# Performance work log

Measured on AMD Instinct MI355X. Metric: run time of the kernel, lower is better.

## Reference

```python
import jax, jax.numpy as jnp
import numpy as np

NUM_HEADS = 4
SPATIAL_DS = 2
EPS = 1e-5


def setup_inputs() -> dict:
    key = jax.random.key(0)
    ks = jax.random.split(key, 6)
    B, C, H, W = 8, 256, 64, 64
    hd = C // NUM_HEADS
    return {
        "x": jax.random.normal(ks[0], (B, C, H, W), jnp.float32),
        "gn_w": jnp.ones((C,), jnp.float32),
        "gn_b": jnp.zeros((C,), jnp.float32),
        "wq": jax.random.normal(ks[1], (C, C), jnp.float32) * (C ** -0.5),
        "wk": jax.random.normal(ks[2], (hd, C), jnp.float32) * (C ** -0.5),
        "wv": jax.random.normal(ks[3], (hd, C), jnp.float32) * (C ** -0.5),
        "wo": jax.random.normal(ks[4], (C, C), jnp.float32) * (C ** -0.5),
        "gamma": jnp.full((C,), 1e-4, jnp.float32),
    }


def reference(x, gn_w, gn_b, wq, wk, wv, wo, gamma):
    B, C, H, W = x.shape
    hd = C // NUM_HEADS
    scale = hd ** -0.5
    ds = SPATIAL_DS

    # GroupNorm with 1 group: normalize over (C,H,W) per sample, per-channel affine
    mu = jnp.mean(x, axis=(1, 2, 3), keepdims=True)
    var = jnp.var(x, axis=(1, 2, 3), keepdims=True)
    xn = (x - mu) * jax.lax.rsqrt(var + EPS)
    xn = xn * gn_w[None, :, None, None] + gn_b[None, :, None, None]

    # Q projection (1x1 conv == channel matmul): (B, heads, N, hd)
    q = jnp.einsum('oc,bchw->bohw', wq, xn).reshape(B, NUM_HEADS, hd, H * W)
    q = jnp.swapaxes(q, 2, 3)  # (B, h, N, hd)

    # AvgPool2d(ds, ds) on normalized input for K/V
    Hd, Wd = H // ds, W // ds
    x_ds = xn.reshape(B, C, Hd, ds, Wd, ds).mean(axis=(3, 5))

    k = jnp.einsum('oc,bchw->bohw', wk, x_ds).reshape(B, hd, Hd * Wd)
    k = jnp.swapaxes(k, 1, 2)  # (B, M, hd) single shared head
    v = jnp.einsum('oc,bchw->bohw', wv, x_ds).reshape(B, hd, Hd * Wd)
    v = jnp.swapaxes(v, 1, 2)  # (B, M, hd)

    # Multi-query attention: queries per-head, shared K/V
    attn = jnp.einsum('bhnd,bmd->bhnm', q, k) * scale
    attn = jax.nn.softmax(attn, axis=-1)
    out = jnp.einsum('bhnm,bmd->bhnd', attn, v)  # (B, h, N, hd)

    out = jnp.swapaxes(out, 2, 3).reshape(B, C, H, W)
    out = jnp.einsum('oc,bchw->bohw', wo, out)

    return x + out * gamma[None, :, None, None]
```

## Files before the change

### kernel.cpp

```cpp
#include <hip/hip_runtime.h>


#define CNT_INV (1.0f/1048576.0f)
#define EPSV 1e-5f
#define QSCALE 0.18033688f

#define WS_STATS 0
#define WS_XNT   64
#define WS_K     5242944
#define WS_V     5505088
#define WS_WQB   5767232
#define WS_WKV   5800000
#define WS_WOB   5816384

typedef __attribute__((ext_vector_type(8))) short bf8_t;
typedef __attribute__((ext_vector_type(4))) float f4_t;

static __device__ __forceinline__ unsigned fbits(float f) {
  union { float f; unsigned u; } v; v.f = f; return v.u;
}
static __device__ __forceinline__ unsigned short f2bf(float f) {
  unsigned u = fbits(f);
  return (unsigned short)((u + 0x7fffu + ((u >> 16) & 1u)) >> 16);
}
static __device__ __forceinline__ unsigned pk_rnd(float a, float b) {
  return __builtin_amdgcn_perm(fbits(b) + 0x8000u, fbits(a) + 0x8000u, 0x07060302u);
}
static __device__ __forceinline__ unsigned pk_tr(float a, float b) {
  return __builtin_amdgcn_perm(fbits(b), fbits(a), 0x07060302u);
}
static __device__ __forceinline__ float bf2f(unsigned short h) {
  union { unsigned u; float f; } v; v.u = ((unsigned)h) << 16; return v.f;
}
static __device__ __forceinline__ float fexp2(float x) {
  float r; asm("v_exp_f32 %0, %1" : "=v"(r) : "v"(x)); return r;
}

static __device__ __forceinline__ bf8_t affine8(bf8_t r, const float* a8, const float* b8) {
  union { bf8_t v; unsigned short u[8]; unsigned w[4]; } in, out;
  in.v = r;
#pragma unroll
  for (int i = 0; i < 4; ++i) {
    float lo = fmaf(bf2f(in.u[2 * i]),     a8[2 * i],     b8[2 * i]);
    float hi = fmaf(bf2f(in.u[2 * i + 1]), a8[2 * i + 1], b8[2 * i + 1]);
    out.w[i] = pk_rnd(lo, hi);
  }
  return out.v;
}

static __device__ __forceinline__ bf8_t pool_affine(bf8_t s00, bf8_t s01, bf8_t s10, bf8_t s11,
                                                    const float* a4, const float* b8) {
  union { bf8_t v; unsigned short u[8]; unsigned w[4]; } x00, x01, x10, x11, out;
  x00.v = s00; x01.v = s01; x10.v = s10; x11.v = s11;
#pragma unroll
  for (int i = 0; i < 4; ++i) {
    float lo = (bf2f(x00.u[2 * i]) + bf2f(x01.u[2 * i])) +
               (bf2f(x10.u[2 * i]) + bf2f(x11.u[2 * i]));
    float hi = (bf2f(x00.u[2 * i + 1]) + bf2f(x01.u[2 * i + 1])) +
               (bf2f(x10.u[2 * i + 1]) + bf2f(x11.u[2 * i + 1]));
    lo = fmaf(lo, a4[2 * i],     b8[2 * i]);
    hi = fmaf(hi, a4[2 * i + 1], b8[2 * i + 1]);
    out.w[i] = pk_rnd(lo, hi);
  }
  return out.v;
}

__global__ __launch_bounds__(256) void k_prep(const float* __restrict__ x,
                                              const float* __restrict__ wq,
                                              const float* __restrict__ wk,
                                              const float* __restrict__ wv,
                                              const float* __restrict__ wo,
                                              float* __restrict__ stats,
                                              unsigned short* __restrict__ wqb,
                                              unsigned short* __restrict__ wkvb,
                                              unsigned short* __restrict__ wob,
                                              unsigned short* __restrict__ xtb) {
  __shared__ unsigned short T[128][72];
  __shared__ float red[8];
  const int blk = blockIdx.x;
  const int t = threadIdx.x;
  if (blk < 512) {
    const int b = blk >> 6;
    const int chunk = blk & 63;
    const float4* xb = (const float4*)(x + (size_t)b * 1048576 + (size_t)chunk * 16384);
    float s = 0.f, s2 = 0.f;
#pragma unroll
    for (int it = 0; it < 16; ++it) {
      float4 v = xb[it * 256 + t];
      s  += v.x + v.y + v.z + v.w;
      s2 += v.x * v.x + v.y * v.y + v.z * v.z + v.w * v.w;
    }
#pragma unroll
    for (int o = 32; o > 0; o >>= 1) {
      s  += __shfl_down(s, o);
      s2 += __shfl_down(s2, o);
    }
    const int wid = t >> 6;
    if ((t & 63) == 0) { red[wid] = s; red[4 + wid] = s2; }
    __syncthreads();
    if (t == 0) {
      atomicAdd(&stats[b * 2 + 0], red[0] + red[1] + red[2] + red[3]);
      atomicAdd(&stats[b * 2 + 1], red[4] + red[5] + red[6] + red[7]);
    }
  } else if (blk < 1152) {
    const int idx = (blk - 512) * 256 + t;
    if (idx < 65536) wqb[idx] = f2bf(wq[idx]);
    else if (idx < 81920) wkvb[idx - 65536] = f2bf(wk[idx - 65536]);
    else if (idx < 98304) wkvb[idx - 65536] = f2bf(wv[idx - 81920]);
    else if (idx < 163840) wob[idx - 98304] = f2bf(wo[idx - 98304]);
  } else {
    const int idx = blk - 1152;
    const int hp = idx & 31, cq = (idx >> 5) & 3, b = idx >> 7;
    const int c0 = cq * 64, n0 = hp * 128;
    const int n4 = (t & 31) * 4, cl = t >> 5;
    const int wswz = t & 7;
#pragma unroll
    for (int p = 0; p < 8; ++p) {
      const int c = c0 + p * 8 + cl;
      const int pc = (p ^ wswz) * 8 + cl;
      float4 v = *(const float4*)&x[(size_t)(b * 256 + c) * 4096 + n0 + n4];
      T[n4 + 0][pc] = f2bf(v.x);
      T[n4 + 1][pc] = f2bf(v.y);
      T[n4 + 2][pc] = f2bf(v.z);
      T[n4 + 3][pc] = f2bf(v.w);
    }
    __syncthreads();
    {
      const int r = t >> 1, cb4 = (t & 1) * 4;
      const int rswz = (t >> 3) & 7;
      unsigned short* dst = xtb + ((size_t)b * 4096 + n0 + r) * 256 + c0 + cb4 * 8;
#pragma unroll
      for (int u = 0; u < 4; ++u)
        *(uint4*)(dst + u * 8) = *(const uint4*)&T[r][((cb4 + u) ^ rswz) * 8];
    }
  }
}

__global__ __launch_bounds__(256) void k_gemm_kv(const unsigned short* __restrict__ wkvb,
                                                 const unsigned short* __restrict__ xtb,
                                                 const float* __restrict__ gnw,
                                                 const float* __restrict__ gnb,
                                                 const float* __restrict__ stats,
                                                 unsigned short* __restrict__ kbf,
                                                 unsigned short* __restrict__ vtbf) {
  __shared__ __align__(16) unsigned short kv0[32][72];
  __shared__ __align__(16) unsigned short kv1[64][40];
  const int t = threadIdx.x;
  const int w = t >> 6, l = t & 63, lane16 = l & 15, quad = l >> 4;
  const int m0 = blockIdx.x * 32, b = blockIdx.y;
  const int kvsel = w >> 1, wh = w & 1;
  const float mu = stats[b * 2 + 0] * CNT_INV;
  const float rstd = rsqrtf(stats[b * 2 + 1] * CNT_INV - mu * mu + EPSV);

  const unsigned short* Abase = wkvb + (size_t)kvsel * 16384 +
                                (size_t)(wh * 32 + lane16) * 256 + quad * 8;
  const unsigned short* B00[2];
#pragma unroll
  for (int mg = 0; mg < 2; ++mg) {
    const int m = m0 + mg * 16 + lane16;
    const int nb = (m >> 5) * 128 + (m & 31) * 2;
    B00[mg] = xtb + ((size_t)b * 4096 + nb) * 256 + quad * 8;
  }

  f4_t acc[2][2];
#pragma unroll
  for (int i = 0; i < 2; ++i)
#pragma unroll
    for (int j = 0; j < 2; ++j) acc[i][j] = (f4_t){0.f, 0.f, 0.f, 0.f};

  for (int kc = 0; kc < 256; kc += 32) {
    const int cb = kc + quad * 8;
    float4 g0 = *(const float4*)&gnw[cb];
    float4 g1 = *(const float4*)&gnw[cb + 4];
    float4 h0 = *(const float4*)&gnb[cb];
    float4 h1 = *(const float4*)&gnb[cb + 4];
    float a4[8], b8[8];
    const float gg[8] = {g0.x, g0.y, g0.z, g0.w, g1.x, g1.y, g1.z, g1.w};
    const float hh[8] = {h0.x, h0.y, h0.z, h0.w, h1.x, h1.y, h1.z, h1.w};
#pragma unroll
    for (int j = 0; j < 8; ++j) {
      const float a = gg[j] * rstd;
      a4[j] = a * 0.25f;
      b8[j] = hh[j] - mu * a;
    }
    bf8_t Bf[2];
#pragma unroll
    for (int mg = 0; mg < 2; ++mg) {
      const unsigned short* p = B00[mg] + kc;
      bf8_t s00 = *(const bf8_t*)p;
      bf8_t s01 = *(const bf8_t*)(p + 256);
      bf8_t s10 = *(const bf8_t*)(p + 64 * 256);
      bf8_t s11 = *(const bf8_t*)(p + 65 * 256);
      Bf[mg] = pool_affine(s00, s01, s10, s11, a4, b8);
    }
    bf8_t A[2];
#pragma unroll
    for (int og = 0; og < 2; ++og) A[og] = *(const bf8_t*)(Abase + (size_t)og * 16 * 256 + kc);
#pragma unroll
    for (int og = 0; og < 2; ++og)
#pragma unroll
      for (int mg = 0; mg < 2; ++mg)
        acc[og][mg] = __builtin_amdgcn_mfma_f32_16x16x32_bf16(A[og], Bf[mg], acc[og][mg], 0, 0, 0);
  }

  if (w < 2) {
#pragma unroll
    for (int og = 0; og < 2; ++og)
#pragma unroll
      for (int mg = 0; mg < 2; ++mg) {
        uint2 p;
        p.x = pk_rnd(acc[og][mg][0], acc[og][mg][1]);
        p.y = pk_rnd(acc[og][mg][2], acc[og][mg][3]);
        *(uint2*)&kv0[mg * 16 + lane16][wh * 32 + og * 16 + quad * 4] = p;
      }
  } else {
#pragma unroll
    for (int og = 0; og < 2; ++og)
#pragma unroll
      for (int mg = 0; mg < 2; ++mg) {
        const int d0 = wh * 32 + og * 16 + quad * 4;
#pragma unroll
        for (int r = 0; r < 4; ++r)
          kv1[d0 + r][mg * 16 + lane16] = f2bf(acc[og][mg][r]);
      }
  }
  __syncthreads();
  {
    const int rowk = t >> 3, ch = t & 7, e = rowk & 7;
    *(uint4*)(kbf + (size_t)b * 65536 + (size_t)(m0 + rowk) * 64 + ((ch ^ e) * 8)) =
        *(const uint4*)&kv0[rowk][ch * 8];
    const int rowd = t >> 2, q = t & 3;
    *(uint4*)(vtbf + (size_t)b * 65536 + (size_t)(m0 >> 5) * 2048 + (size_t)rowd * 32 + q * 8) =
        *(const uint4*)&kv1[rowd][q * 8];
  }
}

__global__ __launch_bounds__(256) void k_fused(const unsigned short* __restrict__ wqb,
                                               const unsigned short* __restrict__ xtb,
                                               const float* __restrict__ gnw,
                                               const float* __restrict__ gnb,
                                               const float* __restrict__ stats,
                                               const unsigned short* __restrict__ kbf,
                                               const unsigned short* __restrict__ vtbf,
                                               const unsigned short* __restrict__ wob,
                                               const float* __restrict__ x,
                                               const float* __restrict__ gamma,
                                               float* __restrict__ outp) {
  __shared__ __align__(16) unsigned short smem[20480];
  __shared__ __align__(16) unsigned short kst[2][2048];
  __shared__ __align__(16) unsigned short vst[2][2048];
  const int t = threadIdx.x;
  const int w = t >> 6, l = t & 63, lane16 = l & 15, quad = l >> 4;
  const int n0 = blockIdx.x * 64, b = blockIdx.y;
  const int h = w;
  unsigned short* qst = smem + w * 4608;
  unsigned short (*plds)[64][40] = (unsigned short (*)[64][40])(smem + w * 5120);
  unsigned short (*aos)[264] = (unsigned short (*)[264])smem;

  const float mu = stats[b * 2 + 0] * CNT_INV;
  const float rstd = rsqrtf(stats[b * 2 + 1] * CNT_INV - mu * mu + EPSV);

  const int sw = w & 1;
  const unsigned short* sbase = (w < 2) ? (kbf + (size_t)b * 65536) : (vtbf + (size_t)b * 65536);
  unsigned short* sdst0 = ((w < 2) ? &kst[0][0] : &vst[0][0]) + sw * 1024 + l * 8;
  unsigned short* sdst1 = ((w < 2) ? &kst[1][0] : &vst[1][0]) + sw * 1024 + l * 8;

#define STAGE_ISSUE(WIN, R0, R1)                                              \
  { const unsigned short* sp = sbase + (size_t)(WIN) * 2048 + sw * 1024 + l * 8; \
    R0 = *(const uint4*)sp; R1 = *(const uint4*)(sp + 512); }
#define STAGE_WRITE(DP, R0, R1)                                               \
  { *(uint4*)(DP) = R0; *(uint4*)((DP) + 512) = R1; }

#define READ_K(BUF, KREG)                                                     \
  {                                                                           \
    _Pragma("unroll")                                                         \
    for (int s = 0; s < 2; ++s) {                                             \
      _Pragma("unroll")                                                       \
      for (int dc = 0; dc < 2; ++dc)                                          \
        KREG[s][dc] = *(const bf8_t*)&kst[BUF][(s * 16 + lane16) * 64 +       \
                                              (((dc * 4 + quad) ^ (lane16 & 7)) * 8)]; \
    }                                                                         \
  }
#define READ_V(BUF, VREG)                                                     \
  {                                                                           \
    _Pragma("unroll")                                                         \
    for (int dg = 0; dg < 4; ++dg)                                            \
      VREG[dg] = *(const bf8_t*)&vst[BUF][(dg * 16 + lane16) * 32 + quad * 8]; \
  }

  {
    const unsigned short* Abase = wqb + (size_t)(h * 64 + lane16) * 256 + quad * 8;
    const unsigned short* Bbase = xtb + ((size_t)b * 4096 + n0 + lane16) * 256 + quad * 8;
    f4_t qacc[4][4];
#pragma unroll
    for (int i = 0; i < 4; ++i)
#pragma unroll
      for (int j = 0; j < 4; ++j) qacc[i][j] = (f4_t){0.f, 0.f, 0.f, 0.f};
    for (int kc = 0; kc < 256; kc += 32) {
      const int cb = kc + quad * 8;
      float4 g0 = *(const float4*)&gnw[cb];
      float4 g1 = *(const float4*)&gnw[cb + 4];
      float4 h0 = *(const float4*)&gnb[cb];
      float4 h1 = *(const float4*)&gnb[cb + 4];
      float a8[8], b8[8];
      const float gg[8] = {g0.x, g0.y, g0.z, g0.w, g1.x, g1.y, g1.z, g1.w};
      const float hh[8] = {h0.x, h0.y, h0.z, h0.w, h1.x, h1.y, h1.z, h1.w};
#pragma unroll
      for (int j = 0; j < 8; ++j) {
        a8[j] = gg[j] * rstd;
        b8[j] = hh[j] - mu * a8[j];
      }
      bf8_t A[4], Bf[4];
#pragma unroll
      for (int og = 0; og < 4; ++og) A[og] = *(const bf8_t*)(Abase + (size_t)og * 16 * 256 + kc);
#pragma unroll
      for (int ng = 0; ng < 4; ++ng) {
        bf8_t raw = *(const bf8_t*)(Bbase + (size_t)ng * 16 * 256 + kc);
        Bf[ng] = affine8(raw, a8, b8);
      }
#pragma unroll
      for (int og = 0; og < 4; ++og)
#pragma unroll
        for (int ng = 0; ng < 4; ++ng)
          qacc[og][ng] = __builtin_amdgcn_mfma_f32_16x16x32_bf16(A[og], Bf[ng], qacc[og][ng], 0, 0, 0);
    }
#pragma unroll
    for (int og = 0; og < 4; ++og)
#pragma unroll
      for (int ng = 0; ng < 4; ++ng) {
        uint2 p;
        p.x = pk_rnd(qacc[og][ng][0] * QSCALE, qacc[og][ng][1] * QSCALE);
        p.y = pk_rnd(qacc[og][ng][2] * QSCALE, qacc[og][ng][3] * QSCALE);
        *(uint2*)&qst[(ng * 16 + lane16) * 72 + og * 16 + quad * 4] = p;
      }
  }
  bf8_t Qf[4][2];
#pragma unroll
  for (int qg = 0; qg < 4; ++qg)
#pragma unroll
    for (int dc = 0; dc < 2; ++dc)
      Qf[qg][dc] = *(const bf8_t*)&qst[(qg * 16 + lane16) * 72 + dc * 32 + quad * 8];
  __syncthreads();

  f4_t O[4][4];
#pragma unroll
  for (int dg = 0; dg < 4; ++dg)
#pragma unroll
    for (int qg = 0; qg < 4; ++qg) O[dg][qg] = (f4_t){0.f, 0.f, 0.f, 0.f};
  f4_t O4[4];
#pragma unroll
  for (int qg = 0; qg < 4; ++qg) O4[qg] = (f4_t){0.f, 0.f, 0.f, 0.f};
  const short onebf = (lane16 == 0) ? (short)0x3F80 : (short)0;
  const bf8_t Aone = {onebf, onebf, onebf, onebf, onebf, onebf, onebf, onebf};

#define SSTEP(KREG, BUF)                                                      \
  {                                                                           \
    _Pragma("unroll")                                                         \
    for (int qg = 0; qg < 4; ++qg) {                                          \
      _Pragma("unroll")                                                       \
      for (int s = 0; s < 2; ++s) {                                           \
        f4_t S = (f4_t){0.f, 0.f, 0.f, 0.f};                                  \
        S = __builtin_amdgcn_mfma_f32_16x16x32_bf16(KREG[s][0], Qf[qg][0], S, 0, 0, 0); \
        S = __builtin_amdgcn_mfma_f32_16x16x32_bf16(KREG[s][1], Qf[qg][1], S, 0, 0, 0); \
        float e0 = fexp2(S[0]);                                               \
        float e1 = fexp2(S[1]);                                               \
        float e2 = fexp2(S[2]);                                               \
        float e3 = fexp2(S[3]);                                               \
        uint2 p; p.x = pk_tr(e0, e1); p.y = pk_tr(e2, e3);                    \
        *(uint2*)&plds[BUF][qg * 16 + lane16][s * 16 + quad * 4] = p;         \
      }                                                                       \
    }                                                                         \
  }

  {
    uint4 a0, a1, b0, b1;
    STAGE_ISSUE(0, a0, a1);
    STAGE_ISSUE(1, b0, b1);
    STAGE_WRITE(sdst0, a0, a1);
    STAGE_WRITE(sdst1, b0, b1);
  }
  __syncthreads();

  bf8_t Kc[2][2], Vc[4];
  READ_K(0, Kc);
  SSTEP(Kc, 0);
  READ_V(0, Vc);
  __syncthreads();

  for (int it = 1; it < 32; ++it) {
    const int cur = it & 1, pb = cur ^ 1;
    uint4 g0, g1;
    if (it < 31) STAGE_ISSUE(it + 1, g0, g1);
    bf8_t Pf[4];
#pragma unroll
    for (int qg = 0; qg < 4; ++qg)
      Pf[qg] = *(const bf8_t*)&plds[pb][qg * 16 + lane16][quad * 8];
    READ_K(cur, Kc);
    bf8_t Vn[4];
    READ_V(cur, Vn);
    __builtin_amdgcn_s_setprio(1);
#pragma unroll
    for (int dg = 0; dg < 4; ++dg)
#pragma unroll
      for (int qg = 0; qg < 4; ++qg)
        O[dg][qg] = __builtin_amdgcn_mfma_f32_16x16x32_bf16(Vc[dg], Pf[qg], O[dg][qg], 0, 0, 0);
#pragma unroll
    for (int qg = 0; qg < 4; ++qg)
      O4[qg] = __builtin_amdgcn_mfma_f32_16x16x32_bf16(Aone, Pf[qg], O4[qg], 0, 0, 0);
    __builtin_amdgcn_s_setprio(0);
    SSTEP(Kc, cur);
#pragma unroll
    for (int dg = 0; dg < 4; ++dg) Vc[dg] = Vn[dg];
    if (it < 31) STAGE_WRITE((cur ? sdst0 : sdst1), g0, g1);
    __syncthreads();
  }
  {
    bf8_t Pf[4];
#pragma unroll
    for (int qg = 0; qg < 4; ++qg)
      Pf[qg] = *(const bf8_t*)&plds[1][qg * 16 + lane16][quad * 8];
    __builtin_amdgcn_s_setprio(1);
#pragma unroll
    for (int dg = 0; dg < 4; ++dg)
#pragma unroll
      for (int qg = 0; qg < 4; ++qg)
        O[dg][qg] = __builtin_amdgcn_mfma_f32_16x16x32_bf16(Vc[dg], Pf[qg], O[dg][qg], 0, 0, 0);
#pragma unroll
    for (int qg = 0; qg < 4; ++qg)
      O4[qg] = __builtin_amdgcn_mfma_f32_16x16x32_bf16(Aone, Pf[qg], O4[qg], 0, 0, 0);
    __builtin_amdgcn_s_setprio(0);
  }
#undef SSTEP
#undef STAGE_ISSUE
#undef STAGE_WRITE
#undef READ_K
#undef READ_V

  float rden[4];
#pragma unroll
  for (int qg = 0; qg < 4; ++qg) {
    float d = __shfl(O4[qg][0], lane16);
    rden[qg] = 1.f / d;
  }

  __syncthreads();
#pragma unroll
  for (int dg = 0; dg < 4; ++dg)
#pragma unroll
    for (int qg = 0; qg < 4; ++qg) {
      const int c0 = h * 64 + dg * 16 + quad * 4;
      uint2 p;
      p.x = pk_rnd(O[dg][qg][0] * rden[qg], O[dg][qg][1] * rden[qg]);
      p.y = pk_rnd(O[dg][qg][2] * rden[qg], O[dg][qg][3] * rden[qg]);
      *(uint2*)&aos[qg * 16 + lane16][c0] = p;
    }
  __syncthreads();

  {
    const unsigned short* Wbase = wob + (size_t)(w * 64 + lane16) * 256 + quad * 8;
    f4_t acc[4][4];
#pragma unroll
    for (int i = 0; i < 4; ++i)
#pragma unroll
      for (int j = 0; j < 4; ++j) acc[i][j] = (f4_t){0.f, 0.f, 0.f, 0.f};
    for (int kc = 0; kc < 256; kc += 32) {
      bf8_t A[4], Bf[4];
#pragma unroll
      for (int og = 0; og < 4; ++og) A[og] = *(const bf8_t*)(Wbase + (size_t)og * 16 * 256 + kc);
#pragma unroll
      for (int ng = 0; ng < 4; ++ng) Bf[ng] = *(const bf8_t*)&aos[ng * 16 + lane16][kc + quad * 8];
#pragma unroll
      for (int og = 0; og < 4; ++og)
#pragma unroll
        for (int ng = 0; ng < 4; ++ng)
          acc[og][ng] = __builtin_amdgcn_mfma_f32_16x16x32_bf16(A[og], Bf[ng], acc[og][ng], 0, 0, 0);
    }
#pragma unroll
    for (int og = 0; og < 4; ++og) {
      float4 g4 = *(const float4*)&gamma[w * 64 + og * 16 + quad * 4];
      const float g[4] = {g4.x, g4.y, g4.z, g4.w};
#pragma unroll
      for (int ng = 0; ng < 4; ++ng) {
        const int n = n0 + ng * 16 + lane16;
#pragma unroll
        for (int r = 0; r < 4; ++r) {
          const int o = w * 64 + og * 16 + quad * 4 + r;
          const size_t ix = ((size_t)(b * 256 + o)) * 4096 + n;
          outp[ix] = x[ix] + g[r] * acc[og][ng][r];
        }
      }
    }
  }
}

extern "C" void kernel_launch(void* const* d_in, const int* in_sizes, int n_in,
                              void* d_out, int out_size, void* d_ws, size_t ws_size,
                              hipStream_t stream) {
  const float* x     = (const float*)d_in[0];
  const float* gnw   = (const float*)d_in[1];
  const float* gnb   = (const float*)d_in[2];
  const float* wq    = (const float*)d_in[3];
  const float* wk    = (const float*)d_in[4];
  const float* wv    = (const float*)d_in[5];
  const float* wo    = (const float*)d_in[6];
  const float* gamma = (const float*)d_in[7];
  float* out = (float*)d_out;
  float* ws  = (float*)d_ws;
  unsigned short* xtb  = (unsigned short*)(ws + WS_XNT);
  unsigned short* kbf  = (unsigned short*)(ws + WS_K);
  unsigned short* vtbf = (unsigned short*)(ws + WS_V);
  unsigned short* wqb  = (unsigned short*)(ws + WS_WQB);
  unsigned short* wkvb = (unsigned short*)(ws + WS_WKV);
  unsigned short* wob  = (unsigned short*)(ws + WS_WOB);

  hipMemsetAsync(ws, 0, 256, stream);
  k_prep<<<2176, 256, 0, stream>>>(x, wq, wk, wv, wo, ws + WS_STATS, wqb, wkvb, wob, xtb);
  k_gemm_kv<<<dim3(32, 8), 256, 0, stream>>>(wkvb, xtb, gnw, gnb, ws + WS_STATS, kbf, vtbf);
  k_fused<<<dim3(64, 8), 256, 0, stream>>>(wqb, xtb, gnw, gnb, ws + WS_STATS, kbf, vtbf, wob, x, gamma, out);
}
```

Before: 201.3 us.

## Fuse all stages into one cooperative kernel with grid-wide syncs

Measured after the change: 441.8 us. 2.19x slower.

```diff
diff --git a/kernel.cpp b/kernel.cpp
--- a/kernel.cpp
+++ b/kernel.cpp
@@ -1,4 +1,7 @@
 #include <hip/hip_runtime.h>
+#include <hip/hip_cooperative_groups.h>
+
+namespace cg = cooperative_groups;
 
 
 #define CNT_INV (1.0f/1048576.0f)
@@ -63,6 +66,413 @@
     out.w[i] = pk_rnd(lo, hi);
   }
   return out.v;
+}
+
+__global__ __launch_bounds__(256) void k_all(const float* __restrict__ x,
+                                             const float* __restrict__ gnw,
+                                             const float* __restrict__ gnb,
+                                             const float* __restrict__ wq,
+                                             const float* __restrict__ wk,
+                                             const float* __restrict__ wv,
+                                             const float* __restrict__ wo,
+                                             const float* __restrict__ gamma,
+                                             float* __restrict__ stats,
+                                             unsigned short* __restrict__ wqb,
+                                             unsigned short* __restrict__ wkvb,
+                                             unsigned short* __restrict__ wob,
+                                             unsigned short* __restrict__ xtb,
+                                             unsigned short* __restrict__ kbf,
+                                             unsigned short* __restrict__ vtbf,
+                                             float* __restrict__ outp) {
+  __shared__ __align__(16) unsigned short smem[20480];
+  __shared__ __align__(16) unsigned short kst[2][2048];
+  __shared__ __align__(16) unsigned short vst[2][2048];
+  __shared__ float red[8];
+  cg::grid_group grid = cg::this_grid();
+  const int t = threadIdx.x;
+  const int bid = blockIdx.x;
+  const int b = bid >> 6, nt = bid & 63;
+  const int w = t >> 6, l = t & 63, lane16 = l & 15, quad = l >> 4;
+
+  {
+    unsigned short (*T)[72] = (unsigned short (*)[72])smem;
+    float s = 0.f, s2 = 0.f;
+    const int n4 = (t & 31) * 4, cl = t >> 5;
+    const int wswz = t & 7;
+    for (int sub = 0; sub < 2; ++sub) {
+      const int tile = nt * 2 + sub;
+      const int c0 = (tile >> 5) * 64, n0a = (tile & 31) * 128;
+#pragma unroll
+      for (int p = 0; p < 8; ++p) {
+        const int c = c0 + p * 8 + cl;
+        const int pc = (p ^ wswz) * 8 + cl;
+        float4 v = *(const float4*)&x[(size_t)(b * 256 + c) * 4096 + n0a + n4];
+        s  += (v.x + v.y) + (v.z + v.w);
+        s2 += (v.x * v.x + v.y * v.y) + (v.z * v.z + v.w * v.w);
+        T[n4 + 0][pc] = f2bf(v.x);
+        T[n4 + 1][pc] = f2bf(v.y);
+        T[n4 + 2][pc] = f2bf(v.z);
+        T[n4 + 3][pc] = f2bf(v.w);
+      }
+      __syncthreads();
+      {
+        const int r = t >> 1, cb4 = (t & 1) * 4;
+        const int rswz = (t >> 3) & 7;
+        unsigned short* dst = xtb + ((size_t)b * 4096 + n0a + r) * 256 + c0 + cb4 * 8;
+#pragma unroll
+        for (int u = 0; u < 4; ++u)
+          *(uint4*)(dst + u * 8) = *(const uint4*)&T[r][((cb4 + u) ^ rswz) * 8];
+      }
+      __syncthreads();
+    }
+#pragma unroll
+    for (int o = 32; o > 0; o >>= 1) {
+      s  += __shfl_down(s, o);
+      s2 += __shfl_down(s2, o);
+    }
+    if ((t & 63) == 0) { red[w] = s; red[4 + w] = s2; }
+    __syncthreads();
+    if (t == 0) {
+      atomicAdd(&stats[b * 2 + 0], red[0] + red[1] + red[2] + red[3]);
+      atomicAdd(&stats[b * 2 + 1], red[4] + red[5] + red[6] + red[7]);
+    }
+    const int base = bid * 320;
+    for (int k = t; k < 320; k += 256) {
+      const int idx = base + k;
+      if (idx < 65536) wqb[idx] = f2bf(wq[idx]);
+      else if (idx < 81920) wkvb[idx - 65536] = f2bf(wk[idx - 65536]);
+      else if (idx < 98304) wkvb[idx - 65536] = f2bf(wv[idx - 81920]);
+      else wob[idx - 98304] = f2bf(wo[idx - 98304]);
+    }
+  }
+  __threadfence();
+  grid.sync();
+
+  const float mu = stats[b * 2 + 0] * CNT_INV;
+  const float rstd = rsqrtf(stats[b * 2 + 1] * CNT_INV - mu * mu + EPSV);
+
+  if (nt < 32) {
+    unsigned short (*kv0)[72] = (unsigned short (*)[72])(&kst[0][0]);
+    unsigned short (*kv1)[40] = (unsigned short (*)[40])(&vst[0][0]);
+    const int m0 = nt * 32;
+    const int kvsel = w >> 1, wh = w & 1;
+    const unsigned short* Abase = wkvb + (size_t)kvsel * 16384 +
+                                  (size_t)(wh * 32 + lane16) * 256 + quad * 8;
+    const unsigned short* B00[2];
+#pragma unroll
+    for (int mg = 0; mg < 2; ++mg) {
+      const int m = m0 + mg * 16 + lane16;
+      const int nb = (m >> 5) * 128 + (m & 31) * 2;
+      B00[mg] = xtb + ((size_t)b * 4096 + nb) * 256 + quad * 8;
+    }
+    f4_t acc[2][2];
+#pragma unroll
+    for (int i = 0; i < 2; ++i)
+#pragma unroll
+      for (int j = 0; j < 2; ++j) acc[i][j] = (f4_t){0.f, 0.f, 0.f, 0.f};
+    for (int kc = 0; kc < 256; kc += 32) {
+      const int cb = kc + quad * 8;
+      float4 g0 = *(const float4*)&gnw[cb];
+      float4 g1 = *(const float4*)&gnw[cb + 4];
+      float4 h0 = *(const float4*)&gnb[cb];
+      float4 h1 = *(const float4*)&gnb[cb + 4];
+      float a4[8], b8[8];
+      const float gg[8] = {g0.x, g0.y, g0.z, g0.w, g1.x, g1.y, g1.z, g1.w};
+      const float hh[8] = {h0.x, h0.y, h0.z, h0.w, h1.x, h1.y, h1.z, h1.w};
+#pragma unroll
+      for (int j = 0; j < 8; ++j) {
+        const float a = gg[j] * rstd;
+        a4[j] = a * 0.25f;
+        b8[j] = hh[j] - mu * a;
+      }
+      bf8_t Bf[2];
+#pragma unroll
+      for (int mg = 0; mg < 2; ++mg) {
+        const unsigned short* p = B00[mg] + kc;
+        bf8_t s00 = *(const bf8_t*)p;
+        bf8_t s01 = *(const bf8_t*)(p + 256);
+        bf8_t s10 = *(const bf8_t*)(p + 64 * 256);
+        bf8_t s11 = *(const bf8_t*)(p + 65 * 256);
+        Bf[mg] = pool_affine(s00, s01, s10, s11, a4, b8);
+      }
+      bf8_t A[2];
+#pragma unroll
+      for (int og = 0; og < 2; ++og) A[og] = *(const bf8_t*)(Abase + (size_t)og * 16 * 256 + kc);
+#pragma unroll
+      for (int og = 0; og < 2; ++og)
+#pragma unroll
+        for (int mg = 0; mg < 2; ++mg)
+          acc[og][mg] = __builtin_amdgcn_mfma_f32_16x16x32_bf16(A[og], Bf[mg], acc[og][mg], 0, 0, 0);
+    }
+    if (w < 2) {
+#pragma unroll
+      for (int og = 0; og < 2; ++og)
+#pragma unroll
+        for (int mg = 0; mg < 2; ++mg) {
+          uint2 p;
+          p.x = pk_rnd(acc[og][mg][0], acc[og][mg][1]);
+          p.y = pk_rnd(acc[og][mg][2], acc[og][mg][3]);
+          *(uint2*)&kv0[mg * 16 + lane16][wh * 32 + og * 16 + quad * 4] = p;
+        }
+    } else {
+#pragma unroll
+      for (int og = 0; og < 2; ++og)
+#pragma unroll
+        for (int mg = 0; mg < 2; ++mg) {
+          const int d0 = wh * 32 + og * 16 + quad * 4;
+#pragma unroll
+          for (int r = 0; r < 4; ++r)
+            kv1[d0 + r][mg * 16 + lane16] = f2bf(acc[og][mg][r]);
+        }
+    }
+    __syncthreads();
+    {
+      const int rowk = t >> 3, ch = t & 7, e = rowk & 7;
+      *(uint4*)(kbf + (size_t)b * 65536 + (size_t)(m0 + rowk) * 64 + ((ch ^ e) * 8)) =
+          *(const uint4*)&kv0[rowk][ch * 8];
+      const int rowd = t >> 2, q = t & 3;
+      *(uint4*)(vtbf + (size_t)b * 65536 + (size_t)nt * 2048 + (size_t)rowd * 32 + q * 8) =
+          *(const uint4*)&kv1[rowd][q * 8];
+    }
+    __syncthreads();
+  }
+
+  const int n0 = nt * 64;
+  const int h = w;
+  unsigned short* qst = smem + w * 4608;
+  unsigned short (*plds)[64][40] = (unsigned short (*)[64][40])(smem + w * 5120);
+  unsigned short (*aos)[264] = (unsigned short (*)[264])smem;
+  {
+    const unsigned short* Abase = wqb + (size_t)(h * 64 + lane16) * 256 + quad * 8;
+    const unsigned short* Bbase = xtb + ((size_t)b * 4096 + n0 + lane16) * 256 + quad * 8;
+    f4_t qacc[4][4];
+#pragma unroll
+    for (int i = 0; i < 4; ++i)
+#pragma unroll
+      for (int j = 0; j < 4; ++j) qacc[i][j] = (f4_t){0.f, 0.f, 0.f, 0.f};
+    for (int kc = 0; kc < 256; kc += 32) {
+      const int cb = kc + quad * 8;
+      float4 g0 = *(const float4*)&gnw[cb];
+      float4 g1 = *(const float4*)&gnw[cb + 4];
+      float4 h0 = *(const float4*)&gnb[cb];
+      float4 h1 = *(const float4*)&gnb[cb + 4];
+      float a8[8], b8[8];
+      const float gg[8] = {g0.x, g0.y, g0.z, g0.w, g1.x, g1.y, g1.z, g1.w};
+      const float hh[8] = {h0.x, h0.y, h0.z, h0.w, h1.x, h1.y, h1.z, h1.w};
+#pragma unroll
+      for (int j = 0; j < 8; ++j) {
+        a8[j] = gg[j] * rstd;
+        b8[j] = hh[j] - mu * a8[j];
+      }
+      bf8_t A[4], Bf[4];
+#pragma unroll
+      for (int og = 0; og < 4; ++og) A[og] = *(const bf8_t*)(Abase + (size_t)og * 16 * 256 + kc);
+#pragma unroll
+      for (int ng = 0; ng < 4; ++ng) {
+        bf8_t raw = *(const bf8_t*)(Bbase + (size_t)ng * 16 * 256 + kc);
+        Bf[ng] = affine8(raw, a8, b8);
+      }
+#pragma unroll
+      for (int og = 0; og < 4; ++og)
+#pragma unroll
+        for (int ng = 0; ng < 4; ++ng)
+          qacc[og][ng] = __builtin_amdgcn_mfma_f32_16x16x32_bf16(A[og], Bf[ng], qacc[og][ng], 0, 0, 0);
+    }
+#pragma unroll
+    for (int og = 0; og < 4; ++og)
+#pragma unroll
+      for (int ng = 0; ng < 4; ++ng) {
+        uint2 p;
+        p.x = pk_rnd(qacc[og][ng][0] * QSCALE, qacc[og][ng][1] * QSCALE);
+        p.y = pk_rnd(qacc[og][ng][2] * QSCALE, qacc[og][ng][3] * QSCALE);
+        *(uint2*)&qst[(ng * 16 + lane16) * 72 + og * 16 + quad * 4] = p;
+      }
+  }
+  bf8_t Qf[4][2];
+#pragma unroll
+  for (int qg = 0; qg < 4; ++qg)
+#pragma unroll
+    for (int dc = 0; dc < 2; ++dc)
+      Qf[qg][dc] = *(const bf8_t*)&qst[(qg * 16 + lane16) * 72 + dc * 32 + quad * 8];
+  __syncthreads();
+  __threadfence();
+  grid.sync();
+
+  const int sw = w & 1;
+  const unsigned short* sbase = (w < 2) ? (kbf + (size_t)b * 65536) : (vtbf + (size_t)b * 65536);
+  unsigned short* sdst0 = ((w < 2) ? &kst[0][0] : &vst[0][0]) + sw * 1024 + l * 8;
+  unsigned short* sdst1 = ((w < 2) ? &kst[1][0] : &vst[1][0]) + sw * 1024 + l * 8;
+
+#define STAGE_ISSUE(WIN, R0, R1)                                              \
+  { const unsigned short* sp = sbase + (size_t)(WIN) * 2048 + sw * 1024 + l * 8; \
+    R0 = *(const uint4*)sp; R1 = *(const uint4*)(sp + 512); }
+#define STAGE_WRITE(DP, R0, R1)                                               \
+  { *(uint4*)(DP) = R0; *(uint4*)((DP) + 512) = R1; }
+#define READ_K(BUF, KREG)                                                     \
+  {                                                                           \
+    _Pragma("unroll")                                                         \
+    for (int s = 0; s < 2; ++s) {                                             \
+      _Pragma("unroll")                                                       \
+      for (int dc = 0; dc < 2; ++dc)                                          \
+        KREG[s][dc] = *(const bf8_t*)&kst[BUF][(s * 16 + lane16) * 64 +       \
+                                              (((dc * 4 + quad) ^ (lane16 & 7)) * 8)]; \
+    }                                                                         \
+  }
+#define READ_V(BUF, VREG)                                                     \
+  {                                                                           \
+    _Pragma("unroll")                                                         \
+    for (int dg = 0; dg < 4; ++dg)                                            \
+      VREG[dg] = *(const bf8_t*)&vst[BUF][(dg * 16 + lane16) * 32 + quad * 8]; \
+  }
+#define SSTEP(KREG, BUF)                                                      \
+  {                                                                           \
+    _Pragma("unroll")                                                         \
+    for (int qg = 0; qg < 4; ++qg) {                                          \
+      _Pragma("unroll")                                                       \
+      for (int s = 0; s < 2; ++s) {                                           \
+        f4_t S = (f4_t){0.f, 0.f, 0.f, 0.f};                                  \
+        S = __builtin_amdgcn_mfma_f32_16x16x32_bf16(KREG[s][0], Qf[qg][0], S, 0, 0, 0); \
+        S = __builtin_amdgcn_mfma_f32_16x16x32_bf16(KREG[s][1], Qf[qg][1], S, 0, 0, 0); \
+        float e0 = fexp2(S[0]);                                               \
+        float e1 = fexp2(S[1]);                                               \
+        float e2 = fexp2(S[2]);                                               \
+        float e3 = fexp2(S[3]);                                               \
+        uint2 p; p.x = pk_tr(e0, e1); p.y = pk_tr(e2, e3);                    \
+        *(uint2*)&plds[BUF][qg * 16 + lane16][s * 16 + quad * 4] = p;         \
+      }                                                                       \
+    }                                                                         \
+  }
+
+  f4_t O[4][4];
+#pragma unroll
+  for (int dg = 0; dg < 4; ++dg)
+#pragma unroll
+    for (int qg = 0; qg < 4; ++qg) O[dg][qg] = (f4_t){0.f, 0.f, 0.f, 0.f};
+  f4_t O4[4];
+#pragma unroll
+  for (int qg = 0; qg < 4; ++qg) O4[qg] = (f4_t){0.f, 0.f, 0.f, 0.f};
+  const short onebf = (lane16 == 0) ? (short)0x3F80 : (short)0;
+  const bf8_t Aone = {onebf, onebf, onebf, onebf, onebf, onebf, onebf, onebf};
+
+  {
+    uint4 a0, a1, b0, b1;
+    STAGE_ISSUE(0, a0, a1);
+    STAGE_ISSUE(1, b0, b1);
+    STAGE_WRITE(sdst0, a0, a1);
+    STAGE_WRITE(sdst1, b0, b1);
+  }
+  __syncthreads();
+
+  bf8_t Kc[2][2], Vc[4];
+  READ_K(0, Kc);
+  SSTEP(Kc, 0);
+  READ_V(0, Vc);
+  __syncthreads();
+
+  for (int it = 1; it < 32; ++it) {
+    const int cur = it & 1, pb = cur ^ 1;
+    uint4 g0, g1;
+    if (it < 31) STAGE_ISSUE(it + 1, g0, g1);
+    bf8_t Pf[4];
+#pragma unroll
+    for (int qg = 0; qg < 4; ++qg)
+      Pf[qg] = *(const bf8_t*)&plds[pb][qg * 16 + lane16][quad * 8];
+    READ_K(cur, Kc);
+    bf8_t Vn[4];
+    READ_V(cur, Vn);
+    __builtin_amdgcn_s_setprio(1);
+#pragma unroll
+    for (int dg = 0; dg < 4; ++dg)
+#pragma unroll
+      for (int qg = 0; qg < 4; ++qg)
+        O[dg][qg] = __builtin_amdgcn_mfma_f32_16x16x32_bf16(Vc[dg], Pf[qg], O[dg][qg], 0, 0, 0);
+#pragma unroll
+    for (int qg = 0; qg < 4; ++qg)
+      O4[qg] = __builtin_amdgcn_mfma_f32_16x16x32_bf16(Aone, Pf[qg], O4[qg], 0, 0, 0);
+    __builtin_amdgcn_s_setprio(0);
+    SSTEP(Kc, cur);
+#pragma unroll
+    for (int dg = 0; dg < 4; ++dg) Vc[dg] = Vn[dg];
+    if (it < 31) STAGE_WRITE((cur ? sdst0 : sdst1), g0, g1);
+    __syncthreads();
+  }
+  {
+    bf8_t Pf[4];
+#pragma unroll
+    for (int qg = 0; qg < 4; ++qg)
+      Pf[qg] = *(const bf8_t*)&plds[1][qg * 16 + lane16][quad * 8];
+    __builtin_amdgcn_s_setprio(1);
+#pragma unroll
+    for (int dg = 0; dg < 4; ++dg)
+#pragma unroll
+      for (int qg = 0; qg < 4; ++qg)
+        O[dg][qg] = __builtin_amdgcn_mfma_f32_16x16x32_bf16(Vc[dg], Pf[qg], O[dg][qg], 0, 0, 0);
+#pragma unroll
+    for (int qg = 0; qg < 4; ++qg)
+      O4[qg] = __builtin_amdgcn_mfma_f32_16x16x32_bf16(Aone, Pf[qg], O4[qg], 0, 0, 0);
+    __builtin_amdgcn_s_setprio(0);
+  }
+#undef SSTEP
+#undef STAGE_ISSUE
+#undef STAGE_WRITE
+#undef READ_K
+#undef READ_V
+
+  float rden[4];
+#pragma unroll
+  for (int qg = 0; qg < 4; ++qg) {
+    float d = __shfl(O4[qg][0], lane16);
+    rden[qg] = 1.f / d;
+  }
+
+  __syncthreads();
+#pragma unroll
+  for (int dg = 0; dg < 4; ++dg)
+#pragma unroll
+    for (int qg = 0; qg < 4; ++qg) {
+      const int c0 = h * 64 + dg * 16 + quad * 4;
+      uint2 p;
+      p.x = pk_rnd(O[dg][qg][0] * rden[qg], O[dg][qg][1] * rden[qg]);
+      p.y = pk_rnd(O[dg][qg][2] * rden[qg], O[dg][qg][3] * rden[qg]);
+      *(uint2*)&aos[qg * 16 + lane16][c0] = p;
+    }
+  __syncthreads();
+
+  {
+    const unsigned short* Wbase = wob + (size_t)(w * 64 + lane16) * 256 + quad * 8;
+    f4_t acc[4][4];
+#pragma unroll
+    for (int i = 0; i < 4; ++i)
+#pragma unroll
+      for (int j = 0; j < 4; ++j) acc[i][j] = (f4_t){0.f, 0.f, 0.f, 0.f};
+    for (int kc = 0; kc < 256; kc += 32) {
+      bf8_t A[4], Bf[4];
+#pragma unroll
+      for (int og = 0; og < 4; ++og) A[og] = *(const bf8_t*)(Wbase + (size_t)og * 16 * 256 + kc);
+#pragma unroll
+      for (int ng = 0; ng < 4; ++ng) Bf[ng] = *(const bf8_t*)&aos[ng * 16 + lane16][kc + quad * 8];
+#pragma unroll
+      for (int og = 0; og < 4; ++og)
+#pragma unroll
+        for (int ng = 0; ng < 4; ++ng)
+          acc[og][ng] = __builtin_amdgcn_mfma_f32_16x16x32_bf16(A[og], Bf[ng], acc[og][ng], 0, 0, 0);
+    }
+#pragma unroll
+    for (int og = 0; og < 4; ++og) {
+      float4 g4 = *(const float4*)&gamma[w * 64 + og * 16 + quad * 4];
+      const float g[4] = {g4.x, g4.y, g4.z, g4.w};
+#pragma unroll
+      for (int ng = 0; ng < 4; ++ng) {
+        const int n = n0 + ng * 16 + lane16;
+#pragma unroll
+        for (int r = 0; r < 4; ++r) {
+          const int o = w * 64 + og * 16 + quad * 4 + r;
+          const size_t ix = ((size_t)(b * 256 + o)) * 4096 + n;
+          outp[ix] = x[ix] + g[r] * acc[og][ng][r];
+        }
+      }
+    }
+  }
 }
 
 __global__ __launch_bounds__(256) void k_prep(const float* __restrict__ x,
@@ -151,7 +561,6 @@
   const int kvsel = w >> 1, wh = w & 1;
   const float mu = stats[b * 2 + 0] * CNT_INV;
   const float rstd = rsqrtf(stats[b * 2 + 1] * CNT_INV - mu * mu + EPSV);
-
   const unsigned short* Abase = wkvb + (size_t)kvsel * 16384 +
                                 (size_t)(wh * 32 + lane16) * 256 + quad * 8;
   const unsigned short* B00[2];
@@ -161,13 +570,11 @@
     const int nb = (m >> 5) * 128 + (m & 31) * 2;
     B00[mg] = xtb + ((size_t)b * 4096 + nb) * 256 + quad * 8;
   }
-
   f4_t acc[2][2];
 #pragma unroll
   for (int i = 0; i < 2; ++i)
 #pragma unroll
     for (int j = 0; j < 2; ++j) acc[i][j] = (f4_t){0.f, 0.f, 0.f, 0.f};
-
   for (int kc = 0; kc < 256; kc += 32) {
     const int cb = kc + quad * 8;
     float4 g0 = *(const float4*)&gnw[cb];
@@ -202,7 +609,6 @@
       for (int mg = 0; mg < 2; ++mg)
         acc[og][mg] = __builtin_amdgcn_mfma_f32_16x16x32_bf16(A[og], Bf[mg], acc[og][mg], 0, 0, 0);
   }
-
   if (w < 2) {
 #pragma unroll
     for (int og = 0; og < 2; ++og)
@@ -256,10 +662,8 @@
   unsigned short* qst = smem + w * 4608;
   unsigned short (*plds)[64][40] = (unsigned short (*)[64][40])(smem + w * 5120);
   unsigned short (*aos)[264] = (unsigned short (*)[264])smem;
-
   const float mu = stats[b * 2 + 0] * CNT_INV;
   const float rstd = rsqrtf(stats[b * 2 + 1] * CNT_INV - mu * mu + EPSV);
-
   const int sw = w & 1;
   const unsigned short* sbase = (w < 2) ? (kbf + (size_t)b * 65536) : (vtbf + (size_t)b * 65536);
   unsigned short* sdst0 = ((w < 2) ? &kst[0][0] : &vst[0][0]) + sw * 1024 + l * 8;
@@ -270,7 +674,6 @@
     R0 = *(const uint4*)sp; R1 = *(const uint4*)(sp + 512); }
 #define STAGE_WRITE(DP, R0, R1)                                               \
   { *(uint4*)(DP) = R0; *(uint4*)((DP) + 512) = R1; }
-
 #define READ_K(BUF, KREG)                                                     \
   {                                                                           \
     _Pragma("unroll")                                                         \
@@ -287,72 +690,6 @@
     for (int dg = 0; dg < 4; ++dg)                                            \
       VREG[dg] = *(const bf8_t*)&vst[BUF][(dg * 16 + lane16) * 32 + quad * 8]; \
   }
-
-  {
-    const unsigned short* Abase = wqb + (size_t)(h * 64 + lane16) * 256 + quad * 8;
-    const unsigned short* Bbase = xtb + ((size_t)b * 4096 + n0 + lane16) * 256 + quad * 8;
-    f4_t qacc[4][4];
-#pragma unroll
-    for (int i = 0; i < 4; ++i)
-#pragma unroll
-      for (int j = 0; j < 4; ++j) qacc[i][j] = (f4_t){0.f, 0.f, 0.f, 0.f};
-    for (int kc = 0; kc < 256; kc += 32) {
-      const int cb = kc + quad * 8;
-      float4 g0 = *(const float4*)&gnw[cb];
-      float4 g1 = *(const float4*)&gnw[cb + 4];
-      float4 h0 = *(const float4*)&gnb[cb];
-      float4 h1 = *(const float4*)&gnb[cb + 4];
-      float a8[8], b8[8];
-      const float gg[8] = {g0.x, g0.y, g0.z, g0.w, g1.x, g1.y, g1.z, g1.w};
-      const float hh[8] = {h0.x, h0.y, h0.z, h0.w, h1.x, h1.y, h1.z, h1.w};
-#pragma unroll
-      for (int j = 0; j < 8; ++j) {
-        a8[j] = gg[j] * rstd;
-        b8[j] = hh[j] - mu * a8[j];
-      }
-      bf8_t A[4], Bf[4];
-#pragma unroll
-      for (int og = 0; og < 4; ++og) A[og] = *(const bf8_t*)(Abase + (size_t)og * 16 * 256 + kc);
-#pragma unroll
-      for (int ng = 0; ng < 4; ++ng) {
-        bf8_t raw = *(const bf8_t*)(Bbase + (size_t)ng * 16 * 256 + kc);
-        Bf[ng] = affine8(raw, a8, b8);
-      }
-#pragma unroll
-      for (int og = 0; og < 4; ++og)
-#pragma unroll
-        for (int ng = 0; ng < 4; ++ng)
-          qacc[og][ng] = __builtin_amdgcn_mfma_f32_16x16x32_bf16(A[og], Bf[ng], qacc[og][ng], 0, 0, 0);
-    }
-#pragma unroll
-    for (int og = 0; og < 4; ++og)
-#pragma unroll
-      for (int ng = 0; ng < 4; ++ng) {
-        uint2 p;
-        p.x = pk_rnd(qacc[og][ng][0] * QSCALE, qacc[og][ng][1] * QSCALE);
-        p.y = pk_rnd(qacc[og][ng][2] * QSCALE, qacc[og][ng][3] * QSCALE);
-        *(uint2*)&qst[(ng * 16 + lane16) * 72 + og * 16 + quad * 4] = p;
-      }
-  }
-  bf8_t Qf[4][2];
-#pragma unroll
-  for (int qg = 0; qg < 4; ++qg)
-#pragma unroll
-    for (int dc = 0; dc < 2; ++dc)
-      Qf[qg][dc] = *(const bf8_t*)&qst[(qg * 16 + lane16) * 72 + dc * 32 + quad * 8];
-  __syncthreads();
-
-  f4_t O[4][4];
-#pragma unroll
-  for (int dg = 0; dg < 4; ++dg)
-#pragma unroll
-    for (int qg = 0; qg < 4; ++qg) O[dg][qg] = (f4_t){0.f, 0.f, 0.f, 0.f};
-  f4_t O4[4];
-#pragma unroll
-  for (int qg = 0; qg < 4; ++qg) O4[qg] = (f4_t){0.f, 0.f, 0.f, 0.f};
-  const short onebf = (lane16 == 0) ? (short)0x3F80 : (short)0;
-  const bf8_t Aone = {onebf, onebf, onebf, onebf, onebf, onebf, onebf, onebf};
-
 #define SSTEP(KREG, BUF)                                                      \
   {                                                                           \
     _Pragma("unroll")                                                         \
@@ -373,6 +710,71 @@
   }
 
   {
+    const unsigned short* Abase = wqb + (size_t)(h * 64 + lane16) * 256 + quad * 8;
+    const unsigned short* Bbase = xtb + ((size_t)b * 4096 + n0 + lane16) * 256 + quad * 8;
+    f4_t qacc[4][4];
+#pragma unroll
+    for (int i = 0; i < 4; ++i)
+#pragma unroll
+      for (int j = 0; j < 4; ++j) qacc[i][j] = (f4_t){0.f, 0.f, 0.f, 0.f};
+    for (int kc = 0; kc < 256; kc += 32) {
+      const int cb = kc + quad * 8;
+      float4 g0 = *(const float4*)&gnw[cb];
+      float4 g1 = *(const float4*)&gnw[cb + 4];
+      float4 h0 = *(const float4*)&gnb[cb];
+      float4 h1 = *(const float4*)&gnb[cb + 4];
+      float a8[8], b8[8];
+      const float gg[8] = {g0.x, g0.y, g0.z, g0.w, g1.x, g1.y, g1.z, g1.w};
+      const float hh[8] = {h0.x, h0.y, h0.z, h0.w, h1.x, h1.y, h1.z, h1.w};
+#pragma unroll
+      for (int j = 0; j < 8; ++j) {
+        a8[j] = gg[j] * rstd;
+        b8[j] = hh[j] - mu * a8[j];
+      }
+      bf8_t A[4], Bf[4];
+#pragma unroll
+      for (int og = 0; og < 4; ++og) A[og] = *(const bf8_t*)(Abase + (size_t)og * 16 * 256 + kc);
+#pragma unroll
+      for (int ng = 0; ng < 4; ++ng) {
+        bf8_t raw = *(const bf8_t*)(Bbase + (size_t)ng * 16 * 256 + kc);
+        Bf[ng] = affine8(raw, a8, b8);
+      }
+#pragma unroll
+      for (int og = 0; og < 4; ++og)
+#pragma unroll
+        for (int ng = 0; ng < 4; ++ng)
+          qacc[og][ng] = __builtin_amdgcn_mfma_f32_16x16x32_bf16(A[og], Bf[ng], qacc[og][ng], 0, 0, 0);
+    }
+#pragma unroll
+    for (int og = 0; og < 4; ++og)
+#pragma unroll
+      for (int ng = 0; ng < 4; ++ng) {
+        uint2 p;
+        p.x = pk_rnd(qacc[og][ng][0] * QSCALE, qacc[og][ng][1] * QSCALE);
+        p.y = pk_rnd(qacc[og][ng][2] * QSCALE, qacc[og][ng][3] * QSCALE);
+        *(uint2*)&qst[(ng * 16 + lane16) * 72 + og * 16 + quad * 4] = p;
+      }
+  }
+  bf8_t Qf[4][2];
+#pragma unroll
+  for (int qg = 0; qg < 4; ++qg)
+#pragma unroll
+    for (int dc = 0; dc < 2; ++dc)
+      Qf[qg][dc] = *(const bf8_t*)&qst[(qg * 16 + lane16) * 72 + dc * 32 + quad * 8];
+  __syncthreads();
+
+  f4_t O[4][4];
+#pragma unroll
+  for (int dg = 0; dg < 4; ++dg)
+#pragma unroll
+    for (int qg = 0; qg < 4; ++qg) O[dg][qg] = (f4_t){0.f, 0.f, 0.f, 0.f};
+  f4_t O4[4];
+#pragma unroll
+  for (int qg = 0; qg < 4; ++qg) O4[qg] = (f4_t){0.f, 0.f, 0.f, 0.f};
+  const short onebf = (lane16 == 0) ? (short)0x3F80 : (short)0;
+  const bf8_t Aone = {onebf, onebf, onebf, onebf, onebf, onebf, onebf, onebf};
+
+  {
     uint4 a0, a1, b0, b1;
     STAGE_ISSUE(0, a0, a1);
     STAGE_ISSUE(1, b0, b1);
@@ -506,6 +908,7 @@
   const float* gamma = (const float*)d_in[7];
   float* out = (float*)d_out;
   float* ws  = (float*)d_ws;
+  float* statsp = ws + WS_STATS;
   unsigned short* xtb  = (unsigned short*)(ws + WS_XNT);
   unsigned short* kbf  = (unsigned short*)(ws + WS_K);
   unsigned short* vtbf = (unsigned short*)(ws + WS_V);
@@ -514,7 +917,15 @@
   unsigned short* wob  = (unsigned short*)(ws + WS_WOB);
 
   hipMemsetAsync(ws, 0, 256, stream);
-  k_prep<<<2176, 256, 0, stream>>>(x, wq, wk, wv, wo, ws + WS_STATS, wqb, wkvb, wob, xtb);
-  k_gemm_kv<<<dim3(32, 8), 256, 0, stream>>>(wkvb, xtb, gnw, gnb, ws + WS_STATS, kbf, vtbf);
-  k_fused<<<dim3(64, 8), 256, 0, stream>>>(wqb, xtb, gnw, gnb, ws + WS_STATS, kbf, vtbf, wob, x, gamma, out);
-}
+  void* args[] = {(void*)&x, (void*)&gnw, (void*)&gnb, (void*)&wq, (void*)&wk, (void*)&wv,
+                  (void*)&wo, (void*)&gamma, (void*)&statsp, (void*)&wqb, (void*)&wkvb,
+                  (void*)&wob, (void*)&xtb, (void*)&kbf, (void*)&vtbf, (void*)&out};
+  hipError_t err = hipLaunchCooperativeKernel((void*)k_all, dim3(512), dim3(256),
+                                              args, 0, stream);
+  if (err != hipSuccess) {
+    k_prep<<<2176, 256, 0, stream>>>(x, wq, wk, wv, wo, statsp, wqb, wkvb, wob, xtb);
+    k_gemm_kv<<<dim3(32, 8), 256, 0, stream>>>(wkvb, xtb, gnw, gnb, statsp, kbf, vtbf);
+    k_fused<<<dim3(64, 8), 256, 0, stream>>>(wqb, xtb, gnw, gnb, statsp, kbf, vtbf, wob,
+                                             x, gamma, out);
+  }
+}
```
